# Kernel tuning notes

Measured on AMD Instinct MI355X. Metric: run time of the kernel, lower is better.

The kernel has to match this reference:

```python
import jax, jax.numpy as jnp
import numpy as np

N_HEAD = 8
D_MODEL = 512
D_K = 512
D_V = 512
D_KH = D_K // N_HEAD
D_VH = D_V // N_HEAD
EPS = 1e-6


def setup_inputs() -> dict:
    key = jax.random.key(0)
    ks = jax.random.split(key, 10)
    B, L = 16, 1024
    q = jax.random.normal(ks[0], (B, L, D_MODEL), dtype=jnp.float32)
    k = jax.random.normal(ks[1], (B, L, D_MODEL), dtype=jnp.float32)
    v = jax.random.normal(ks[2], (B, L, D_MODEL), dtype=jnp.float32)
    mask = jax.random.randint(ks[3], (B, L, L), 0, 2).astype(bool)
    s = 1.0 / np.sqrt(D_MODEL)
    Wq = jax.random.normal(ks[4], (D_MODEL, D_K), dtype=jnp.float32) * s
    Wk = jax.random.normal(ks[5], (D_MODEL, D_K), dtype=jnp.float32) * s
    Wv = jax.random.normal(ks[6], (D_MODEL, D_V), dtype=jnp.float32) * s
    Wfc = jax.random.normal(ks[7], (D_V, D_MODEL), dtype=jnp.float32) * (1.0 / np.sqrt(D_V))
    gamma = jnp.ones((D_MODEL,), dtype=jnp.float32)
    beta = jnp.zeros((D_MODEL,), dtype=jnp.float32)
    return {"q": q, "k": k, "v": v, "mask": mask, "Wq": Wq, "Wk": Wk,
            "Wv": Wv, "Wfc": Wfc, "gamma": gamma, "beta": beta}


def reference(q, k, v, mask, Wq, Wk, Wv, Wfc, gamma, beta):
    B, Lq, _ = q.shape
    Lk = k.shape[1]
    residual = q
    # projections -> [B, H, L, d_head]
    qh = (q @ Wq).reshape(B, Lq, N_HEAD, D_KH).transpose(0, 2, 1, 3)
    kh = (k @ Wk).reshape(B, Lk, N_HEAD, D_KH).transpose(0, 2, 1, 3)
    vh = (v @ Wv).reshape(B, Lk, N_HEAD, D_VH).transpose(0, 2, 1, 3)
    # scaled dot-product attention; scale uses per-head dim (source rebinds d_k)
    scores = jnp.einsum('bhqd,bhkd->bhqk', qh / np.sqrt(D_KH), kh)
    scores = jnp.where(mask[:, None, :, :], -1e9, scores)
    attn = jax.nn.softmax(scores, axis=-1)
    out = jnp.einsum('bhqk,bhkd->bhqd', attn, vh)
    out = out.transpose(0, 2, 1, 3).reshape(B, Lq, D_V)
    out = out @ Wfc + residual
    # layer norm
    mu = jnp.mean(out, axis=-1, keepdims=True)
    var = jnp.var(out, axis=-1, keepdims=True)
    out = (out - mu) * jax.lax.rsqrt(var + EPS) * gamma + beta
    return out, attn
```

## Files before the change

### kernel.cpp

```cpp
#include <hip/hip_runtime.h>
#include <hip/hip_bf16.h>

typedef __attribute__((ext_vector_type(8))) short s8v;
typedef __attribute__((ext_vector_type(4))) short s4v;
typedef __attribute__((ext_vector_type(4))) float f4v;

__device__ __forceinline__ short f2bf(float f){
  unsigned u = __builtin_bit_cast(unsigned, f);
  u += 0x7fffu + ((u >> 16) & 1u);
  return (short)(u >> 16);
}

__device__ __forceinline__ f4v mfma16(s8v a, s8v b, f4v c){
  return __builtin_amdgcn_mfma_f32_16x16x32_bf16(a, b, c, 0, 0, 0);
}

__device__ __forceinline__ void ldsbar(){
  asm volatile("s_waitcnt lgkmcnt(0)" ::: "memory");
  __builtin_amdgcn_s_barrier();
  __builtin_amdgcn_sched_barrier(0);
}

#define LOG2E 1.44269504088896f

__global__ __launch_bounds__(256) void prep_kernel(
    const int* __restrict__ mask, unsigned* __restrict__ bits,
    const float* __restrict__ Wq, const float* __restrict__ Wk,
    const float* __restrict__ Wv, const float* __restrict__ Wfc,
    short* __restrict__ Wt)
{
  if (blockIdx.x < 2048){
    const int lane = threadIdx.x & 63;
    const int wid = blockIdx.x*4 + (threadIdx.x >> 6);
    for (int i = 0; i < 32; ++i){
      const int c = wid*32 + i;
      int mv = __builtin_nontemporal_load(&mask[(size_t)c*64 + lane]);
      unsigned long long bal = __ballot(mv != 0);
      if (lane == 0)  bits[c*2]   = (unsigned)bal;
      if (lane == 32) bits[c*2+1] = (unsigned)(bal >> 32);
    }
  } else {
    const int bid = blockIdx.x - 2048;
    const int w = bid >> 10;
    const float* __restrict__ W = (w==0)?Wq:(w==1)?Wk:(w==2)?Wv:Wfc;
    const int idx = (bid & 1023)*256 + threadIdx.x;
    const int kk = idx >> 9, n = idx & 511;
    Wt[w*262144 + n*512 + kk] = f2bf(W[idx]);
  }
}

__global__ __launch_bounds__(256) void proj_kernel(
    const float* __restrict__ qin, const float* __restrict__ kin,
    const float* __restrict__ vin, const short* __restrict__ Wt,
    short* __restrict__ Qh, short* __restrict__ Kh, short* __restrict__ Vt)
{
  const int work = (blockIdx.x & 7)*384 + (blockIdx.x >> 3);
  const int z = work >> 10;
  const int r = work & 1023;
  const int mt = r >> 2, nt = r & 3;
  const float* __restrict__ A = (z==0) ? qin : (z==1) ? kin : vin;
  const short* __restrict__ W = Wt + z*262144;
  const int m0 = mt*64, n0 = nt*128;
  __shared__ __align__(16) short Alds[2][64*40];
  __shared__ __align__(16) short Tlds[128*68];
  const int tid = threadIdx.x, lane = tid & 63, wave = tid >> 6;
  const int wm = wave >> 1, wn = wave & 1;
  const int col = lane & 15, kg = lane >> 4;
  f4v acc[2][4];
  #pragma unroll
  for (int i=0;i<2;i++)
    #pragma unroll
    for (int j=0;j<4;j++) acc[i][j] = (f4v){0.f,0.f,0.f,0.f};

  const int arow = tid >> 2, aoff = (tid & 3)*8;
  const float* Ap = A + (size_t)(m0 + arow)*512 + aoff;

  float4 x0 = *(const float4*)(Ap);
  float4 x1 = *(const float4*)(Ap + 4);
  int buf = 0;

  for (int k0 = 0; k0 < 512; k0 += 32){
    s8v ab;
    ab[0]=f2bf(x0.x); ab[1]=f2bf(x0.y); ab[2]=f2bf(x0.z); ab[3]=f2bf(x0.w);
    ab[4]=f2bf(x1.x); ab[5]=f2bf(x1.y); ab[6]=f2bf(x1.z); ab[7]=f2bf(x1.w);
    *(s8v*)&Alds[buf][arow*40 + aoff] = ab;
    if (k0 < 480){
      x0 = *(const float4*)(Ap + k0 + 32);
      x1 = *(const float4*)(Ap + k0 + 36);
    }
    ldsbar();
    s8v af0 = *(const s8v*)&Alds[buf][(wm*32 + col)*40 + kg*8];
    s8v af1 = *(const s8v*)&Alds[buf][(wm*32 + 16 + col)*40 + kg*8];
    #pragma unroll
    for (int f=0; f<4; f++){
      const int n = n0 + wn*64 + f*16 + col;
      s8v bf = *(const s8v*)(W + n*512 + k0 + kg*8);
      acc[0][f] = mfma16(af0, bf, acc[0][f]);
      acc[1][f] = mfma16(af1, bf, acc[1][f]);
    }
    buf ^= 1;
  }

  if (z < 2){
    const float scale = (z==0) ? 0.125f*LOG2E : 1.0f;
    short* D = (z==0) ? Qh : Kh;
    #pragma unroll
    for (int fr=0; fr<2; fr++)
      #pragma unroll
      for (int f=0; f<4; f++)
        #pragma unroll
        for (int j=0; j<4; j++){
          int rr = m0 + wm*32 + fr*16 + kg*4 + j;
          int c = n0 + wn*64 + f*16 + col;
          int b = rr >> 10, l = rr & 1023, hh = c >> 6, d = c & 63;
          D[((size_t)(b*8+hh)*1024 + l)*64 + d] = f2bf(acc[fr][f][j] * scale);
        }
  } else {
    #pragma unroll
    for (int fr=0; fr<2; fr++)
      #pragma unroll
      for (int f=0; f<4; f++)
        #pragma unroll
        for (int j=0; j<4; j++){
          const int rl = wm*32 + fr*16 + kg*4 + j;
          const int cl = wn*64 + f*16 + col;
          Tlds[cl*68 + rl] = f2bf(acc[fr][f][j]);
        }
    ldsbar();
    const int b = m0 >> 10, lbase = m0 & 1023;
    #pragma unroll
    for (int it=0; it<4; ++it){
      const int idx = it*256 + tid;
      const int cl = idx >> 3, rc = idx & 7;
      const int c = n0 + cl, hh = c >> 6, d = c & 63;
      s8v vv = *(const s8v*)&Tlds[cl*68 + rc*8];
      *(s8v*)(Vt + ((size_t)(b*8+hh)*64 + d)*1024 + lbase + rc*8) = vv;
    }
  }
}

__global__ __launch_bounds__(256) void attn_kernel(
  const short* __restrict__ Qh, const short* __restrict__ Kh,
  const short* __restrict__ Vt, const unsigned* __restrict__ bits,
  float* __restrict__ attn, short* __restrict__ ctx)
{
  const int work = ((blockIdx.x & 7) << 8) | (blockIdx.x >> 3);
  const int bh = work >> 4;
  const int q0 = (work & 15) * 64;
  const int b = bh >> 3, h = bh & 7;
  __shared__ unsigned mb[64*33];
  __shared__ __align__(16) short Pb[64*128];
  __shared__ float red[256];
  __shared__ float rowinv[64];
  const int tid = threadIdx.x, lane = tid & 63, wave = tid >> 6;
  const int col = lane & 15, kg = lane >> 4;
  const short* Qb = Qh + (size_t)bh*65536;
  const short* Kb = Kh + (size_t)bh*65536;
  const short* Vb = Vt + (size_t)bh*65536;
  const f4v zf = (f4v){0.f,0.f,0.f,0.f};

  {
    const int r = tid >> 2, w = (tid & 3)*8;
    const unsigned* src = bits + (size_t)(b*1024 + q0 + r)*32 + w;
    uint4 w0 = *(const uint4*)src;
    uint4 w1 = *(const uint4*)(src + 4);
    unsigned* dst = &mb[r*33 + w];
    dst[0]=w0.x; dst[1]=w0.y; dst[2]=w0.z; dst[3]=w0.w;
    dst[4]=w1.x; dst[5]=w1.y; dst[6]=w1.z; dst[7]=w1.w;
  }

  s8v qf[4][2];
  #pragma unroll
  for (int qi = 0; qi < 4; ++qi)
    #pragma unroll
    for (int ks = 0; ks < 2; ++ks)
      qf[qi][ks] = *(const s8v*)(Qb + (q0 + qi*16 + col)*64 + ks*32 + kg*8);

  __syncthreads();

  float sum[4] = {0.f, 0.f, 0.f, 0.f};
  f4v cacc[4] = {zf, zf, zf, zf};
  const int d0 = wave*16;
  const int sw = (col & 7) << 3;
  for (int it = 0; it < 8; ++it){
    const int c0 = it*128 + wave*32;
    unsigned mw[4];
    #pragma unroll
    for (int qi = 0; qi < 4; ++qi) mw[qi] = mb[(qi*16 + col)*33 + (c0>>5)];
    #pragma unroll
    for (int ch = 0; ch < 2; ++ch){
      const int cc = c0 + ch*16;
      const short* kp = Kb + (cc + col)*64 + kg*8;
      s8v kf0 = *(const s8v*)kp;
      s8v kf1 = *(const s8v*)(kp + 32);
      #pragma unroll
      for (int qi = 0; qi < 4; ++qi){
        f4v a = mfma16(kf0, qf[qi][0], zf);
        a = mfma16(kf1, qf[qi][1], a);
        s4v pk;
        #pragma unroll
        for (int j = 0; j < 4; ++j){
          const int bit = ch*16 + kg*4 + j;
          float e = exp2f(a[j]);
          float p = ((mw[qi]>>bit)&1) ? 0.f : e;
          sum[qi] += p;
          pk[j] = f2bf(p);
        }
        *(s4v*)&Pb[(qi*16 + col)*128 + ((wave*32 + ch*16 + kg*4) ^ sw)] = pk;
      }
    }
    ldsbar();
    #pragma unroll
    for (int sub = 0; sub < 4; ++sub){
      s8v vf = *(const s8v*)(Vb + (size_t)(d0 + col)*1024 + it*128 + sub*32 + kg*8);
      const int kr = (sub*32 + kg*8) ^ sw;
      #pragma unroll
      for (int qi = 0; qi < 4; ++qi){
        s8v pa = *(const s8v*)&Pb[(qi*16 + col)*128 + kr];
        cacc[qi] = mfma16(pa, vf, cacc[qi]);
      }
    }
    ldsbar();
  }

  #pragma unroll
  for (int qi = 0; qi < 4; ++qi){
    sum[qi] += __shfl_xor(sum[qi], 16);
    sum[qi] += __shfl_xor(sum[qi], 32);
  }
  if (kg == 0){
    #pragma unroll
    for (int qi = 0; qi < 4; ++qi) red[wave*64 + qi*16 + col] = sum[qi];
  }
  __syncthreads();
  if (tid < 64)
    rowinv[tid] = 1.0f / (red[tid] + red[64+tid] + red[128+tid] + red[192+tid]);
  __syncthreads();

  short* cb = ctx + (size_t)(b*1024 + q0)*512 + h*64 + d0 + col;
  #pragma unroll
  for (int qi = 0; qi < 4; ++qi)
    #pragma unroll
    for (int j = 0; j < 4; ++j)
      cb[(size_t)(qi*16 + kg*4 + j)*512] =
          f2bf(cacc[qi][j] * rowinv[qi*16 + kg*4 + j]);

  float inv[4];
  #pragma unroll
  for (int qi = 0; qi < 4; ++qi) inv[qi] = rowinv[qi*16 + col];
  float* ab = attn + (size_t)(bh*1024 + q0)*1024;
  for (int it = 0; it < 8; ++it){
    const int c0 = it*128 + wave*32;
    unsigned mw[4];
    #pragma unroll
    for (int qi = 0; qi < 4; ++qi) mw[qi] = mb[(qi*16 + col)*33 + (c0>>5)];
    #pragma unroll
    for (int ch = 0; ch < 2; ++ch){
      const int cc = c0 + ch*16;
      const short* kp = Kb + (cc + col)*64 + kg*8;
      s8v kf0 = *(const s8v*)kp;
      s8v kf1 = *(const s8v*)(kp + 32);
      #pragma unroll
      for (int qi = 0; qi < 4; ++qi){
        f4v a = mfma16(kf0, qf[qi][0], zf);
        a = mfma16(kf1, qf[qi][1], a);
        f4v p;
        #pragma unroll
        for (int j = 0; j < 4; ++j){
          const int bit = ch*16 + kg*4 + j;
          float e = exp2f(a[j]) * inv[qi];
          p[j] = ((mw[qi]>>bit)&1) ? 0.f : e;
        }
        __builtin_nontemporal_store(p,
            (f4v*)(ab + (size_t)(qi*16 + col)*1024 + cc + kg*4));
      }
    }
  }
}

__global__ __launch_bounds__(256) void outproj_ln_kernel(
  const short* __restrict__ ctx, const short* __restrict__ Wf,
  const float* __restrict__ resid, const float* __restrict__ gamma,
  const float* __restrict__ beta, float* __restrict__ out)
{
  const int m0 = blockIdx.x * 32;
  __shared__ __align__(16) short Alds[2][32*40];
  __shared__ float sred[32*4], qred[32*4];
  __shared__ float mLds[32], rLds[32];
  const int tid = threadIdx.x, lane = tid & 63, wave = tid >> 6;
  const int col = lane & 15, kg = lane >> 4;
  const int n0 = wave * 128;

  f4v acc[2][8];
  #pragma unroll
  for (int mf=0; mf<2; mf++)
    #pragma unroll
    for (int nf=0; nf<8; nf++) acc[mf][nf] = (f4v){0.f,0.f,0.f,0.f};

  const int arow = tid >> 3, ac = (tid & 7)*4;
  const short* Ap = ctx + (size_t)(m0 + arow)*512 + ac;

  s4v av = *(const s4v*)(Ap);
  int buf = 0;

  for (int k0 = 0; k0 < 512; k0 += 32){
    *(s4v*)&Alds[buf][arow*40 + ac] = av;
    if (k0 < 480) av = *(const s4v*)(Ap + k0 + 32);
    ldsbar();
    s8v af[2];
    #pragma unroll
    for (int mf=0; mf<2; mf++)
      af[mf] = *(const s8v*)&Alds[buf][(mf*16 + col)*40 + kg*8];
    #pragma unroll
    for (int nf=0; nf<8; nf++){
      s8v bf = *(const s8v*)(Wf + (size_t)(n0 + nf*16 + col)*512 + k0 + kg*8);
      #pragma unroll
      for (int mf=0; mf<2; mf++)
        acc[mf][nf] = mfma16(af[mf], bf, acc[mf][nf]);
    }
    buf ^= 1;
  }

  float g[8], bt[8];
  #pragma unroll
  for (int nf=0; nf<8; nf++){
    g[nf]  = gamma[n0 + nf*16 + col];
    bt[nf] = beta[n0 + nf*16 + col];
  }

  #pragma unroll
  for (int mf=0; mf<2; mf++)
    #pragma unroll
    for (int j=0; j<4; j++){
      const int rl = mf*16 + kg*4 + j;
      const size_t r = (size_t)(m0 + rl);
      float s = 0.f, qq = 0.f;
      #pragma unroll
      for (int nf=0; nf<8; nf++){
        float y = acc[mf][nf][j] + resid[r*512 + n0 + nf*16 + col];
        acc[mf][nf][j] = y;
        s += y; qq += y*y;
      }
      #pragma unroll
      for (int d=1; d<16; d<<=1){ s += __shfl_xor(s, d); qq += __shfl_xor(qq, d); }
      if (col == 0){ sred[rl*4 + wave] = s; qred[rl*4 + wave] = qq; }
    }
  __syncthreads();
  if (tid < 32){
    float S = sred[tid*4] + sred[tid*4+1] + sred[tid*4+2] + sred[tid*4+3];
    float Q = qred[tid*4] + qred[tid*4+1] + qred[tid*4+2] + qred[tid*4+3];
    float mean = S * (1.0f/512.0f);
    float var  = Q * (1.0f/512.0f) - mean*mean;
    mLds[tid] = mean;
    rLds[tid] = rsqrtf(var + 1e-6f);
  }
  __syncthreads();

  #pragma unroll
  for (int mf=0; mf<2; mf++)
    #pragma unroll
    for (int j=0; j<4; j++){
      const int rl = mf*16 + kg*4 + j;
      const size_t r = (size_t)(m0 + rl);
      const float mean = mLds[rl], rs = rLds[rl];
      #pragma unroll
      for (int nf=0; nf<8; nf++)
        out[r*512 + n0 + nf*16 + col] = (acc[mf][nf][j] - mean)*rs*g[nf] + bt[nf];
    }
}

extern "C" void kernel_launch(void* const* d_in, const int* in_sizes, int n_in,
                              void* d_out, int out_size, void* d_ws, size_t ws_size,
                              hipStream_t stream) {
  const float* q    = (const float*)d_in[0];
  const float* k    = (const float*)d_in[1];
  const float* v    = (const float*)d_in[2];
  const int*   mask = (const int*)d_in[3];
  const float* Wq   = (const float*)d_in[4];
  const float* Wk   = (const float*)d_in[5];
  const float* Wv   = (const float*)d_in[6];
  const float* Wfc  = (const float*)d_in[7];
  const float* gamma= (const float*)d_in[8];
  const float* beta = (const float*)d_in[9];

  char* ws = (char*)d_ws;
  short* Wt  = (short*)(ws);
  short* Qh  = (short*)(ws + ((size_t)2<<20));
  short* Kh  = (short*)(ws + ((size_t)18<<20));
  short* Vt  = (short*)(ws + ((size_t)34<<20));
  short* ctx = (short*)(ws + ((size_t)50<<20));

  float* out  = (float*)d_out;
  float* attn = out + (size_t)16384*512;
  unsigned* bits = (unsigned*)d_out;

  prep_kernel<<<dim3(6144,1,1), 256, 0, stream>>>(mask, bits, Wq, Wk, Wv, Wfc, Wt);
  proj_kernel <<<dim3(3072,1,1), 256, 0, stream>>>(q, k, v, Wt, Qh, Kh, Vt);
  attn_kernel <<<dim3(2048,1,1), 256, 0, stream>>>(Qh, Kh, Vt, bits, attn, ctx);
  outproj_ln_kernel<<<dim3(512,1,1), 256, 0, stream>>>(ctx, Wt + 3*262144, q,
                                                       gamma, beta, out);
}
```

Measured before the change: 339.1 us.

## Enlarge projection tile to 128x128 and move mask packing into projection kernel

The projection GEMM now computes 128x128 tiles per block, with each wave holding a 64x64 accumulator, so every B-fragment load feeds four MFMAs instead of two. This halves the projection blocks and cuts redundant weight reads. Mask bit-packing moves from the weight-prep kernel into extra blocks of the projection kernel, so the memory-bound mask read overlaps the GEMM work. The A and transpose LDS buffers are aliased to save shared memory, at the cost of higher register pressure per thread and a shared-memory sized for the larger transpose tile.

```diff
diff --git a/kernel.cpp b/kernel.cpp
--- a/kernel.cpp
+++ b/kernel.cpp
@@ -24,14 +24,26 @@
 #define LOG2E 1.44269504088896f
 
 __global__ __launch_bounds__(256) void prep_kernel(
-    const int* __restrict__ mask, unsigned* __restrict__ bits,
     const float* __restrict__ Wq, const float* __restrict__ Wk,
     const float* __restrict__ Wv, const float* __restrict__ Wfc,
     short* __restrict__ Wt)
 {
-  if (blockIdx.x < 2048){
+  const int w = blockIdx.x >> 10;
+  const float* __restrict__ W = (w==0)?Wq:(w==1)?Wk:(w==2)?Wv:Wfc;
+  const int idx = (blockIdx.x & 1023)*256 + threadIdx.x;
+  const int kk = idx >> 9, n = idx & 511;
+  Wt[w*262144 + n*512 + kk] = f2bf(W[idx]);
+}
+
+__global__ __launch_bounds__(256) void proj_kernel(
+    const float* __restrict__ qin, const float* __restrict__ kin,
+    const float* __restrict__ vin, const short* __restrict__ Wt,
+    const int* __restrict__ mask, unsigned* __restrict__ bits,
+    short* __restrict__ Qh, short* __restrict__ Kh, short* __restrict__ Vt)
+{
+  if (blockIdx.x >= 1536){
     const int lane = threadIdx.x & 63;
-    const int wid = blockIdx.x*4 + (threadIdx.x >> 6);
+    const int wid = (blockIdx.x - 1536)*4 + (threadIdx.x >> 6);
     for (int i = 0; i < 32; ++i){
       const int c = wid*32 + i;
       int mv = __builtin_nontemporal_load(&mask[(size_t)c*64 + lane]);
@@ -39,64 +51,64 @@
       if (lane == 0)  bits[c*2]   = (unsigned)bal;
       if (lane == 32) bits[c*2+1] = (unsigned)(bal >> 32);
     }
-  } else {
-    const int bid = blockIdx.x - 2048;
-    const int w = bid >> 10;
-    const float* __restrict__ W = (w==0)?Wq:(w==1)?Wk:(w==2)?Wv:Wfc;
-    const int idx = (bid & 1023)*256 + threadIdx.x;
-    const int kk = idx >> 9, n = idx & 511;
-    Wt[w*262144 + n*512 + kk] = f2bf(W[idx]);
-  }
-}
-
-__global__ __launch_bounds__(256) void proj_kernel(
-    const float* __restrict__ qin, const float* __restrict__ kin,
-    const float* __restrict__ vin, const short* __restrict__ Wt,
-    short* __restrict__ Qh, short* __restrict__ Kh, short* __restrict__ Vt)
-{
-  const int work = (blockIdx.x & 7)*384 + (blockIdx.x >> 3);
-  const int z = work >> 10;
-  const int r = work & 1023;
+    return;
+  }
+  const int work = (blockIdx.x & 7)*192 + (blockIdx.x >> 3);
+  const int z = work / 512;
+  const int r = work - z*512;
   const int mt = r >> 2, nt = r & 3;
   const float* __restrict__ A = (z==0) ? qin : (z==1) ? kin : vin;
   const short* __restrict__ W = Wt + z*262144;
-  const int m0 = mt*64, n0 = nt*128;
-  __shared__ __align__(16) short Alds[2][64*40];
-  __shared__ __align__(16) short Tlds[128*68];
+  const int m0 = mt*128, n0 = nt*128;
+  __shared__ __align__(16) char smem[34816];
+  short* Alds = (short*)smem;
+  short* Tlds = (short*)smem;
   const int tid = threadIdx.x, lane = tid & 63, wave = tid >> 6;
   const int wm = wave >> 1, wn = wave & 1;
   const int col = lane & 15, kg = lane >> 4;
-  f4v acc[2][4];
-  #pragma unroll
-  for (int i=0;i<2;i++)
+
+  f4v acc[4][4];
+  #pragma unroll
+  for (int i=0;i<4;i++)
     #pragma unroll
     for (int j=0;j<4;j++) acc[i][j] = (f4v){0.f,0.f,0.f,0.f};
 
-  const int arow = tid >> 2, aoff = (tid & 3)*8;
+  const int arow = tid >> 1, aoff = (tid & 1)*16;
   const float* Ap = A + (size_t)(m0 + arow)*512 + aoff;
 
   float4 x0 = *(const float4*)(Ap);
   float4 x1 = *(const float4*)(Ap + 4);
+  float4 x2 = *(const float4*)(Ap + 8);
+  float4 x3 = *(const float4*)(Ap + 12);
   int buf = 0;
 
   for (int k0 = 0; k0 < 512; k0 += 32){
-    s8v ab;
-    ab[0]=f2bf(x0.x); ab[1]=f2bf(x0.y); ab[2]=f2bf(x0.z); ab[3]=f2bf(x0.w);
-    ab[4]=f2bf(x1.x); ab[5]=f2bf(x1.y); ab[6]=f2bf(x1.z); ab[7]=f2bf(x1.w);
-    *(s8v*)&Alds[buf][arow*40 + aoff] = ab;
+    s8v ab0, ab1;
+    ab0[0]=f2bf(x0.x); ab0[1]=f2bf(x0.y); ab0[2]=f2bf(x0.z); ab0[3]=f2bf(x0.w);
+    ab0[4]=f2bf(x1.x); ab0[5]=f2bf(x1.y); ab0[6]=f2bf(x1.z); ab0[7]=f2bf(x1.w);
+    ab1[0]=f2bf(x2.x); ab1[1]=f2bf(x2.y); ab1[2]=f2bf(x2.z); ab1[3]=f2bf(x2.w);
+    ab1[4]=f2bf(x3.x); ab1[5]=f2bf(x3.y); ab1[6]=f2bf(x3.z); ab1[7]=f2bf(x3.w);
+    short* Aw = Alds + buf*5120 + arow*40 + aoff;
+    *(s8v*)Aw = ab0;
+    *(s8v*)(Aw + 8) = ab1;
     if (k0 < 480){
       x0 = *(const float4*)(Ap + k0 + 32);
       x1 = *(const float4*)(Ap + k0 + 36);
-    }
-    ldsbar();
-    s8v af0 = *(const s8v*)&Alds[buf][(wm*32 + col)*40 + kg*8];
-    s8v af1 = *(const s8v*)&Alds[buf][(wm*32 + 16 + col)*40 + kg*8];
+      x2 = *(const float4*)(Ap + k0 + 40);
+      x3 = *(const float4*)(Ap + k0 + 44);
+    }
+    ldsbar();
+    s8v af[4];
+    #pragma unroll
+    for (int fr=0; fr<4; fr++)
+      af[fr] = *(const s8v*)(Alds + buf*5120 + (wm*64 + fr*16 + col)*40 + kg*8);
     #pragma unroll
     for (int f=0; f<4; f++){
       const int n = n0 + wn*64 + f*16 + col;
       s8v bf = *(const s8v*)(W + n*512 + k0 + kg*8);
-      acc[0][f] = mfma16(af0, bf, acc[0][f]);
-      acc[1][f] = mfma16(af1, bf, acc[1][f]);
+      #pragma unroll
+      for (int fr=0; fr<4; fr++)
+        acc[fr][f] = mfma16(af[fr], bf, acc[fr][f]);
     }
     buf ^= 1;
   }
@@ -105,35 +117,36 @@
     const float scale = (z==0) ? 0.125f*LOG2E : 1.0f;
     short* D = (z==0) ? Qh : Kh;
     #pragma unroll
-    for (int fr=0; fr<2; fr++)
+    for (int fr=0; fr<4; fr++)
       #pragma unroll
       for (int f=0; f<4; f++)
         #pragma unroll
         for (int j=0; j<4; j++){
-          int rr = m0 + wm*32 + fr*16 + kg*4 + j;
+          int rr = m0 + wm*64 + fr*16 + kg*4 + j;
           int c = n0 + wn*64 + f*16 + col;
           int b = rr >> 10, l = rr & 1023, hh = c >> 6, d = c & 63;
           D[((size_t)(b*8+hh)*1024 + l)*64 + d] = f2bf(acc[fr][f][j] * scale);
         }
   } else {
-    #pragma unroll
-    for (int fr=0; fr<2; fr++)
+    ldsbar();
+    #pragma unroll
+    for (int fr=0; fr<4; fr++)
       #pragma unroll
       for (int f=0; f<4; f++)
         #pragma unroll
         for (int j=0; j<4; j++){
-          const int rl = wm*32 + fr*16 + kg*4 + j;
+          const int rl = wm*64 + fr*16 + kg*4 + j;
           const int cl = wn*64 + f*16 + col;
-          Tlds[cl*68 + rl] = f2bf(acc[fr][f][j]);
+          Tlds[cl*136 + rl] = f2bf(acc[fr][f][j]);
         }
     ldsbar();
     const int b = m0 >> 10, lbase = m0 & 1023;
     #pragma unroll
-    for (int it=0; it<4; ++it){
+    for (int it=0; it<8; ++it){
       const int idx = it*256 + tid;
-      const int cl = idx >> 3, rc = idx & 7;
+      const int cl = idx >> 4, rc = idx & 15;
       const int c = n0 + cl, hh = c >> 6, d = c & 63;
-      s8v vv = *(const s8v*)&Tlds[cl*68 + rc*8];
+      s8v vv = *(const s8v*)(Tlds + cl*136 + rc*8);
       *(s8v*)(Vt + ((size_t)(b*8+hh)*64 + d)*1024 + lbase + rc*8) = vv;
     }
   }
@@ -394,8 +407,9 @@
   float* attn = out + (size_t)16384*512;
   unsigned* bits = (unsigned*)d_out;
 
-  prep_kernel<<<dim3(6144,1,1), 256, 0, stream>>>(mask, bits, Wq, Wk, Wv, Wfc, Wt);
-  proj_kernel <<<dim3(3072,1,1), 256, 0, stream>>>(q, k, v, Wt, Qh, Kh, Vt);
+  prep_kernel<<<dim3(4096,1,1), 256, 0, stream>>>(Wq, Wk, Wv, Wfc, Wt);
+  proj_kernel <<<dim3(3584,1,1), 256, 0, stream>>>(q, k, v, Wt, mask, bits,
+                                                   Qh, Kh, Vt);
   attn_kernel <<<dim3(2048,1,1), 256, 0, stream>>>(Qh, Kh, Vt, bits, attn, ctx);
   outproj_ln_kernel<<<dim3(512,1,1), 256, 0, stream>>>(ctx, Wt + 3*262144, q,
                                                        gamma, beta, out);
```

Measured after the change: 372.6 us. 9.9% more time.
